# Performance work log

Hardware: AMD Instinct MI355X
Metric: run time of the kernel (lower is better)

## Reference

```python
import jax, jax.numpy as jnp
import numpy as np

DEFAULT_MASK_VALUE = -0.7 * float(jnp.finfo(jnp.dtype('float32')).max)


def setup_inputs() -> dict:
    key = jax.random.key(0)
    k1, k2, k3, k4 = jax.random.split(key, 4)
    B, T, NQ, NKV, D = 2, 2048, 32, 8, 128
    query = jax.random.normal(k1, (B, T, NQ, D), dtype=jnp.float32)
    k = jax.random.normal(k2, (B, T, NKV, D), dtype=jnp.float32)
    v = jax.random.normal(k3, (B, T, NKV, D), dtype=jnp.float32)
    # packed-sequence segment ids: sorted small ints so segments are contiguous
    decoder_segment_ids = jnp.sort(jax.random.randint(k4, (B, T), 0, 4), axis=-1).astype(jnp.int32)
    return {"query": query, "key": k, "value": v, "decoder_segment_ids": decoder_segment_ids}


def _generate_attention_mask(q_seq_len, kv_seq_len, decoder_segment_ids):
    # segment mask: [b, 1, 1, t, s]
    seg = (decoder_segment_ids[:, :, None] == decoder_segment_ids[:, None, :])[:, None, None, :, :]
    # causal mask: [1, 1, 1, t, s]
    row = jax.lax.broadcasted_iota(jnp.int32, (q_seq_len, kv_seq_len), 0)
    col = jax.lax.broadcasted_iota(jnp.int32, (q_seq_len, kv_seq_len), 1)
    causal = (col <= row)[None, None, None, :, :]
    mask = jnp.logical_and(seg, causal)
    return jnp.where(mask, 0.0, DEFAULT_MASK_VALUE)


def _apply_mask_to_logits(logits, mask):
    return jnp.where(mask >= DEFAULT_MASK_VALUE * 0.5, logits, DEFAULT_MASK_VALUE)


def reference(query, key, value, decoder_segment_ids):
    b, t, n, d = query.shape
    n_kv = key.shape[2]
    g = n // n_kv  # query heads per kv head (GQA)
    q = query.reshape(b, t, n_kv, g, d)
    # qk product (no internal sqrt(d) scaling, matching AttentionOp.qk_product)
    logits = jnp.einsum('btkgd,bskd->bkgts', q, key)  # [b, n_kv, g, t, s]
    mask = _generate_attention_mask(t, key.shape[1], decoder_segment_ids)
    logits = _apply_mask_to_logits(logits, mask)
    weights = jax.nn.softmax(logits, axis=-1).astype(query.dtype)
    out = jnp.einsum('bkgts,bskd->btkgd', weights, value)
    return out.reshape(b, t, n, d)
```

## Files before the change

kernel.cpp:

```cpp
#include <hip/hip_runtime.h>


typedef __bf16 bf16x8 __attribute__((ext_vector_type(8)));
typedef __bf16 bf16x2 __attribute__((ext_vector_type(2)));
typedef _Float16 f16x8 __attribute__((ext_vector_type(8)));
typedef float f32x4 __attribute__((ext_vector_type(4)));
typedef unsigned int uint2v __attribute__((ext_vector_type(2)));

#define B_   2
#define T_   2048
#define NQ_  32
#define NKV_ 8
#define D_   128

#define MASKV (-3.0e38f)
#define LOG2E 1.44269504f
#define TILE_US 8192
#define WS_TILES_BYTES ((size_t)B_ * NKV_ * (T_ / 32) * TILE_US * 2)
#define WS_NEED (WS_TILES_BYTES + (size_t)B_ * T_ * 4)

static __device__ __forceinline__ unsigned short f2bf(float x) {
    union { float f; unsigned int u; } c; c.f = x;
    unsigned int r = c.u + 0x7fffu + ((c.u >> 16) & 1u);
    return (unsigned short)(r >> 16);
}

union U8  { unsigned short us[8]; bf16x8 v; };
union H8  { _Float16 h[8]; f16x8 v; };
union PKW { bf16x2 h; unsigned int u; };
union PA4 { unsigned int u[4]; bf16x8 v; };

static __device__ __forceinline__ void pl32swap(unsigned int& a, unsigned int& b) {
#if __has_builtin(__builtin_amdgcn_permlane32_swap)
    uint2v t = __builtin_amdgcn_permlane32_swap(a, b, false, false);
    a = t.x; b = t.y;
#else
    asm("s_nop 1\n\tv_permlane32_swap_b32 %0, %1" : "+v"(a), "+v"(b));
#endif
}
static __device__ __forceinline__ void pl16swap(unsigned int& a, unsigned int& b) {
#if __has_builtin(__builtin_amdgcn_permlane16_swap)
    uint2v t = __builtin_amdgcn_permlane16_swap(a, b, false, false);
    a = t.x; b = t.y;
#else
    asm("s_nop 1\n\tv_permlane16_swap_b32 %0, %1" : "+v"(a), "+v"(b));
#endif
}

__global__ __launch_bounds__(256)
void prep(const float* __restrict__ kg, const float* __restrict__ vg,
          unsigned short* __restrict__ ws)
{
    const int tid = threadIdx.x;
    const int st  = blockIdx.x;
    const int kvh = blockIdx.y;
    const int b   = blockIdx.z;
    unsigned short* base = ws + ((size_t)((b * NKV_ + kvh) * (T_ / 32) + st)) * TILE_US;

    #pragma unroll
    for (int it = 0; it < 2; ++it) {
        int task = tid + it * 256;
        int r = task >> 4, c16 = task & 15;
        const float* kp = kg + (((size_t)(b * T_ + st * 32 + r)) * NKV_ + kvh) * D_ + c16 * 8;
        H8 hu;
        #pragma unroll
        for (int j = 0; j < 8; ++j) hu.h[j] = (_Float16)kp[j];
        int c = c16 >> 2, qd = c16 & 3, hi = r >> 4, ln = r & 15;
        int slot = (c * 2 + hi) * 64 + qd * 16 + ln;
        *(f16x8*)(base + slot * 8) = hu.v;
    }
    #pragma unroll
    for (int it = 0; it < 2; ++it) {
        int task = tid + it * 256;
        int d = task & 127, sc = task >> 7;
        const float* vp = vg + (((size_t)(b * T_ + st * 32 + sc * 8)) * NKV_ + kvh) * D_ + d;
        U8 pk;
        #pragma unroll
        for (int j = 0; j < 8; ++j) pk.us[j] = f2bf(vp[j * (NKV_ * D_)]);
        int slot = (d >> 4) * 64 + sc * 16 + (d & 15);
        *(bf16x8*)(base + 4096 + slot * 8) = pk.v;
    }
}

__global__ __launch_bounds__(256)
void prep_sstart(const int* __restrict__ seg, int* __restrict__ sstart)
{
    int idx = blockIdx.x * 256 + threadIdx.x;
    int b = idx >> 11, t = idx & (T_ - 1);
    const int* sb = seg + b * T_;
    int target = sb[t];
    int lo = 0, hi = t;
    while (lo < hi) { int mid = (lo + hi) >> 1; if (sb[mid] < target) lo = mid + 1; else hi = mid; }
    sstart[idx] = lo;
}

__global__ __launch_bounds__(256)
void attn_fwd(const float* __restrict__ qg,
              const int* __restrict__ sstart,
              const unsigned short* __restrict__ ws,
              float* __restrict__ outg)
{
    const int tid  = threadIdx.x;
    const int wave = tid >> 6;
    const int lane = tid & 63;
    const int qd   = lane >> 4;
    const int ln   = lane & 15;

    const int kvh  = blockIdx.x;
    const int head = kvh * 4 + wave;
    const int j    = blockIdx.y;
    const int b    = blockIdx.z;

    const unsigned short* wsbase =
        ws + ((size_t)((b * NKV_ + kvh) * (T_ / 32))) * TILE_US + lane * 8;

#define LOADKV(KB, VB, tl) do {                                                \
        const unsigned short* _tb = wsbase + (size_t)(tl) * TILE_US;           \
        _Pragma("unroll")                                                      \
        for (int _c = 0; _c < 4; ++_c) {                                       \
            KB[_c][0] = *(const f16x8*)(_tb + (_c * 2 + 0) * 512);             \
            KB[_c][1] = *(const f16x8*)(_tb + (_c * 2 + 1) * 512);             \
        }                                                                      \
        _Pragma("unroll")                                                      \
        for (int _s = 0; _s < 8; ++_s)                                         \
            VB[_s] = *(const bf16x8*)(_tb + 4096 + _s * 512);                  \
    } while (0)

#define COMPUTE(KB, VB, TL) do {                                               \
        const int _s0 = (TL) * 32;                                             \
        f32x4 S0 = {0.f,0.f,0.f,0.f}, S1 = {0.f,0.f,0.f,0.f};                  \
        __builtin_amdgcn_s_setprio(1);                                         \
        _Pragma("unroll")                                                      \
        for (int c = 0; c < 4; ++c) {                                          \
            S0 = __builtin_amdgcn_mfma_f32_16x16x32_f16(KB[c][0], qh[c], S0,0,0,0); \
            S1 = __builtin_amdgcn_mfma_f32_16x16x32_f16(KB[c][1], qh[c], S1,0,0,0); \
            S0 = __builtin_amdgcn_mfma_f32_16x16x32_f16(KB[c][0], ql[c], S0,0,0,0); \
            S1 = __builtin_amdgcn_mfma_f32_16x16x32_f16(KB[c][1], ql[c], S1,0,0,0); \
        }                                                                      \
        __builtin_amdgcn_s_setprio(0);                                         \
        float p0[4], p1[4];                                                    \
        if (_s0 >= wave_rs_max && _s0 + 31 <= wave_row_min) {                  \
            _Pragma("unroll")                                                  \
            for (int r = 0; r < 4; ++r) {                                      \
                p0[r] = exp2f(S0[r]);                                          \
                p1[r] = exp2f(S1[r]);                                          \
            }                                                                  \
        } else {                                                               \
            _Pragma("unroll")                                                  \
            for (int r = 0; r < 4; ++r) {                                      \
                int kv0 = _s0 + qd * 4 + r;                                    \
                int kv1 = kv0 + 16;                                            \
                float sv0 = (kv0 >= rs_l && kv0 <= trow_l) ? S0[r] : MASKV;    \
                float sv1 = (kv1 >= rs_l && kv1 <= trow_l) ? S1[r] : MASKV;    \
                p0[r] = exp2f(sv0);                                            \
                p1[r] = exp2f(sv1);                                            \
            }                                                                  \
        }                                                                      \
        l_lane += (p0[0] + p0[1]) + (p0[2] + p0[3])                            \
                + (p1[0] + p1[1]) + (p1[2] + p1[3]);                           \
        PKW c0, c1, c2, c3;                                                    \
        c0.h = (bf16x2){(__bf16)p0[0], (__bf16)p0[1]};                         \
        c1.h = (bf16x2){(__bf16)p0[2], (__bf16)p0[3]};                         \
        c2.h = (bf16x2){(__bf16)p1[0], (__bf16)p1[1]};                         \
        c3.h = (bf16x2){(__bf16)p1[2], (__bf16)p1[3]};                         \
        unsigned int w0 = c0.u, w1 = c1.u, w2 = c2.u, w3 = c3.u;               \
        pl32swap(w0, w2); pl32swap(w1, w3);                                    \
        pl16swap(w0, w2); pl16swap(w1, w3);                                    \
        PA4 pw; pw.u[0] = w0; pw.u[1] = w1; pw.u[2] = w2; pw.u[3] = w3;        \
        bf16x8 pa = pw.v;                                                      \
        __builtin_amdgcn_s_setprio(1);                                         \
        _Pragma("unroll")                                                      \
        for (int sub = 0; sub < 8; ++sub)                                      \
            O[sub] = __builtin_amdgcn_mfma_f32_16x16x32_bf16(pa, VB[sub], O[sub],0,0,0); \
        __builtin_amdgcn_s_setprio(0);                                         \
    } while (0)

    for (int phase = 0; phase < 2; ++phase) {
        const int chunk = (phase == 0) ? (2 * (int)gridDim.y - 1 - j) : j;
        const int t0 = chunk * 16;

        f16x8 qh[4], ql[4];
        {
            const float* qrow =
                qg + (((size_t)(b * T_ + (t0 + ln)) * NQ_) + head) * D_;
            #pragma unroll
            for (int c = 0; c < 4; ++c) {
                float4 a  = *(const float4*)(qrow + c * 32 + qd * 8);
                float4 b2 = *(const float4*)(qrow + c * 32 + qd * 8 + 4);
                float xs[8] = {a.x, a.y, a.z, a.w, b2.x, b2.y, b2.z, b2.w};
                H8 hu, lu;
                #pragma unroll
                for (int jj = 0; jj < 8; ++jj) {
                    float x = xs[jj] * LOG2E;
                    _Float16 h = (_Float16)x;
                    hu.h[jj] = h;
                    lu.h[jj] = (_Float16)(x - (float)h);
                }
                qh[c] = hu.v; ql[c] = lu.v;
            }
        }

        const int trow_l = t0 + ln;
        const int rs_l   = sstart[b * T_ + trow_l];
        const int wave_rs_max  = sstart[b * T_ + t0 + 15];
        const int wave_row_min = t0;

        const int tile0   = sstart[b * T_ + t0] >> 5;
        const int n_tiles = ((t0 + 15) >> 5) + 1;

        f32x4 O[8];
        #pragma unroll
        for (int k = 0; k < 8; ++k) O[k] = (f32x4){0.f, 0.f, 0.f, 0.f};
        float l_lane = 0.f;

        f16x8  kA[4][2], kB_[4][2];
        bf16x8 vA[8], vB_[8];

        int t = tile0;
        LOADKV(kA, vA, t);
        while (t + 1 < n_tiles) {
            LOADKV(kB_, vB_, t + 1);
            COMPUTE(kA, vA, t);
            if (t + 2 < n_tiles) LOADKV(kA, vA, t + 2);
            COMPUTE(kB_, vB_, t + 1);
            t += 2;
        }
        if (t < n_tiles) COMPUTE(kA, vA, t);

        float l = l_lane;
        l += __shfl_xor(l, 16);
        l += __shfl_xor(l, 32);
        const float invl = 1.0f / l;
        int trow[4];
        float inv[4];
        #pragma unroll
        for (int r = 0; r < 4; ++r) {
            trow[r] = t0 + qd * 4 + r;
            inv[r]  = __shfl(invl, qd * 4 + r);
        }
        #pragma unroll
        for (int sub = 0; sub < 8; ++sub) {
            #pragma unroll
            for (int r = 0; r < 4; ++r) {
                outg[(((size_t)(b * T_ + trow[r]) * NQ_) + head) * D_ + sub * 16 + ln] =
                    O[sub][r] * inv[r];
            }
        }
    }

#undef LOADKV
#undef COMPUTE
}

#define KSTR 136
#define VSTR 40
#define PSTR 40
static __device__ __forceinline__ float bf2f(unsigned short h) {
    union { unsigned int u; float f; } c; c.u = (unsigned int)h << 16; return c.f;
}
__global__ __launch_bounds__(256)
void attn_fwd_fb(const float* __restrict__ qg,
                 const float* __restrict__ kg,
                 const float* __restrict__ vg,
                 const int* __restrict__ seg,
                 float* __restrict__ outg)
{
    __shared__ unsigned short sKh[32 * KSTR];
    __shared__ unsigned short sKl[32 * KSTR];
    __shared__ unsigned short sVt[128 * VSTR];
    __shared__ unsigned short sP[4][16 * PSTR];

    const int tid  = threadIdx.x;
    const int wave = tid >> 6;
    const int lane = tid & 63;
    const int qd   = lane >> 4;
    const int ln   = lane & 15;
    const int t0   = ((int)gridDim.x - 1 - (int)blockIdx.x) * 64;
    const int head = blockIdx.y;
    const int kvh  = head >> 2;
    const int b    = blockIdx.z;

    bf16x8 qh[4], ql[4];
    {
        const float* qrow =
            qg + (((size_t)(b * T_ + (t0 + wave * 16 + ln)) * NQ_) + head) * D_;
        #pragma unroll
        for (int c = 0; c < 4; ++c) {
            float4 a  = *(const float4*)(qrow + c * 32 + qd * 8);
            float4 b2 = *(const float4*)(qrow + c * 32 + qd * 8 + 4);
            float xs[8] = {a.x, a.y, a.z, a.w, b2.x, b2.y, b2.z, b2.w};
            U8 hu, lu;
            #pragma unroll
            for (int j = 0; j < 8; ++j) {
                unsigned short h = f2bf(xs[j]);
                hu.us[j] = h;
                lu.us[j] = f2bf(xs[j] - bf2f(h));
            }
            qh[c] = hu.v; ql[c] = lu.v;
        }
    }
    const int* sb = seg + (size_t)b * T_;
    int qseg[4];
    #pragma unroll
    for (int r = 0; r < 4; ++r) qseg[r] = sb[t0 + wave * 16 + qd * 4 + r];
    int tile0;
    {
        int target = sb[t0];
        int lo = 0, hi = t0;
        while (lo < hi) { int mid = (lo + hi) >> 1; if (sb[mid] < target) lo = mid + 1; else hi = mid; }
        tile0 = lo >> 5;
    }
    f32x4 O[8];
    #pragma unroll
    for (int i = 0; i < 8; ++i) O[i] = (f32x4){0.f, 0.f, 0.f, 0.f};
    float m_prev[4], l_lane[4];
    #pragma unroll
    for (int r = 0; r < 4; ++r) { m_prev[r] = MASKV; l_lane[r] = 0.f; }
    const int n_tiles = t0 / 32 + 2;

    for (int tile = tile0; tile < n_tiles; ++tile) {
        const int s0 = tile * 32;
        __syncthreads();
        #pragma unroll
        for (int it = 0; it < 2; ++it) {
            int task = tid + it * 256;
            int r = task >> 4, d = (task & 15) * 8;
            const float* kp = kg + (((size_t)(b * T_ + s0 + r) * NKV_) + kvh) * D_ + d;
            float4 a  = *(const float4*)(kp);
            float4 b2 = *(const float4*)(kp + 4);
            float xs[8] = {a.x, a.y, a.z, a.w, b2.x, b2.y, b2.z, b2.w};
            U8 hu, lu;
            #pragma unroll
            for (int j = 0; j < 8; ++j) {
                unsigned short h = f2bf(xs[j]);
                hu.us[j] = h;
                lu.us[j] = f2bf(xs[j] - bf2f(h));
            }
            *(bf16x8*)(sKh + r * KSTR + d) = hu.v;
            *(bf16x8*)(sKl + r * KSTR + d) = lu.v;
        }
        #pragma unroll
        for (int it = 0; it < 2; ++it) {
            int task = tid + it * 256;
            int d = task & 127, sg = task >> 7;
            const float* vp = vg + (((size_t)(b * T_ + s0 + sg * 8) * NKV_) + kvh) * D_ + d;
            U8 pk;
            #pragma unroll
            for (int j = 0; j < 8; ++j) pk.us[j] = f2bf(vp[j * (NKV_ * D_)]);
            *(bf16x8*)(sVt + d * VSTR + sg * 8) = pk.v;
        }
        __syncthreads();

        f32x4 S0 = {0.f,0.f,0.f,0.f}, S1 = {0.f,0.f,0.f,0.f};
        #pragma unroll
        for (int c = 0; c < 4; ++c) {
            bf16x8 kh0 = *(const bf16x8*)(sKh + ln * KSTR + c * 32 + qd * 8);
            bf16x8 kh1 = *(const bf16x8*)(sKh + (16 + ln) * KSTR + c * 32 + qd * 8);
            bf16x8 kl0 = *(const bf16x8*)(sKl + ln * KSTR + c * 32 + qd * 8);
            bf16x8 kl1 = *(const bf16x8*)(sKl + (16 + ln) * KSTR + c * 32 + qd * 8);
            S0 = __builtin_amdgcn_mfma_f32_16x16x32_bf16(qh[c], kh0, S0, 0, 0, 0);
            S1 = __builtin_amdgcn_mfma_f32_16x16x32_bf16(qh[c], kh1, S1, 0, 0, 0);
            S0 = __builtin_amdgcn_mfma_f32_16x16x32_bf16(qh[c], kl0, S0, 0, 0, 0);
            S1 = __builtin_amdgcn_mfma_f32_16x16x32_bf16(qh[c], kl1, S1, 0, 0, 0);
            S0 = __builtin_amdgcn_mfma_f32_16x16x32_bf16(ql[c], kh0, S0, 0, 0, 0);
            S1 = __builtin_amdgcn_mfma_f32_16x16x32_bf16(ql[c], kh1, S1, 0, 0, 0);
        }
        const int ks0 = sb[s0 + ln];
        const int ks1 = sb[s0 + 16 + ln];
        float p0[4], p1[4], alpha[4];
        #pragma unroll
        for (int r = 0; r < 4; ++r) {
            const int trow = t0 + wave * 16 + qd * 4 + r;
            float s0v = ((s0 + ln <= trow) && (ks0 == qseg[r])) ? S0[r] : MASKV;
            float s1v = ((s0 + 16 + ln <= trow) && (ks1 == qseg[r])) ? S1[r] : MASKV;
            float mx = fmaxf(s0v, s1v);
            mx = fmaxf(mx, __shfl_xor(mx, 1));
            mx = fmaxf(mx, __shfl_xor(mx, 2));
            mx = fmaxf(mx, __shfl_xor(mx, 4));
            mx = fmaxf(mx, __shfl_xor(mx, 8));
            const float mn = fmaxf(m_prev[r], mx);
            alpha[r] = __expf(m_prev[r] - mn);
            p0[r] = __expf(s0v - mn);
            p1[r] = __expf(s1v - mn);
            l_lane[r] = alpha[r] * l_lane[r] + p0[r] + p1[r];
            m_prev[r] = mn;
        }
        #pragma unroll
        for (int i = 0; i < 8; ++i) {
            O[i][0] *= alpha[0]; O[i][1] *= alpha[1];
            O[i][2] *= alpha[2]; O[i][3] *= alpha[3];
        }
        {
            unsigned short* pw = sP[wave] + (qd * 4) * PSTR + ln;
            #pragma unroll
            for (int r = 0; r < 4; ++r) {
                pw[r * PSTR]      = f2bf(p0[r]);
                pw[r * PSTR + 16] = f2bf(p1[r]);
            }
        }
        asm volatile("s_waitcnt lgkmcnt(0)" ::: "memory");
        bf16x8 pa = *(const bf16x8*)(sP[wave] + ln * PSTR + qd * 8);
        #pragma unroll
        for (int sub = 0; sub < 8; ++sub) {
            bf16x8 bv = *(const bf16x8*)(sVt + (sub * 16 + ln) * VSTR + qd * 8);
            O[sub] = __builtin_amdgcn_mfma_f32_16x16x32_bf16(pa, bv, O[sub], 0, 0, 0);
        }
    }
    float inv[4];
    #pragma unroll
    for (int r = 0; r < 4; ++r) {
        float l = l_lane[r];
        l += __shfl_xor(l, 1);
        l += __shfl_xor(l, 2);
        l += __shfl_xor(l, 4);
        l += __shfl_xor(l, 8);
        inv[r] = 1.0f / l;
    }
    #pragma unroll
    for (int sub = 0; sub < 8; ++sub) {
        #pragma unroll
        for (int r = 0; r < 4; ++r) {
            const int trow = t0 + wave * 16 + qd * 4 + r;
            outg[(((size_t)(b * T_ + trow) * NQ_) + head) * D_ + sub * 16 + ln] =
                O[sub][r] * inv[r];
        }
    }
}

extern "C" void kernel_launch(void* const* d_in, const int* in_sizes, int n_in,
                              void* d_out, int out_size, void* d_ws, size_t ws_size,
                              hipStream_t stream) {
    const float* q  = (const float*)d_in[0];
    const float* k  = (const float*)d_in[1];
    const float* v  = (const float*)d_in[2];
    const int*   sg = (const int*)d_in[3];
    float*       o  = (float*)d_out;
    if (ws_size >= WS_NEED) {
        unsigned short* ws = (unsigned short*)d_ws;
        int* sstart = (int*)((char*)d_ws + WS_TILES_BYTES);
        prep<<<dim3(T_ / 32, NKV_, B_), dim3(256), 0, stream>>>(k, v, ws);
        prep_sstart<<<dim3(B_ * T_ / 256), dim3(256), 0, stream>>>(sg, sstart);
        attn_fwd<<<dim3(NKV_, T_ / 32, B_), dim3(256), 0, stream>>>(q, sstart, ws, o);
    } else {
        attn_fwd_fb<<<dim3(T_ / 64, NQ_, B_), dim3(256), 0, stream>>>(q, k, v, sg, o);
    }
}
```

Baseline: 193.5 us.

## Process two 16-row query groups per wave to reuse each K/V tile

Each wave now handles 32 query rows as two 16-row groups that share every loaded K/V tile, which halves the tile loads per query row. The grid's T dimension is halved to match, and the fast unmasked path is taken only when the whole 32-row block is unmasked. This doubles the accumulator and Q registers, which may lower occupancy, and halves the number of blocks launched. It also coarsens the causal boundary, so more diagonal tiles go through the masked path.

Measured after the change: 205.7 us. 1.06x slower.

```diff
diff --git a/kernel.cpp b/kernel.cpp
--- a/kernel.cpp
+++ b/kernel.cpp
@@ -126,20 +126,19 @@
             VB[_s] = *(const bf16x8*)(_tb + 4096 + _s * 512);                  \
     } while (0)
 
-#define COMPUTE(KB, VB, TL) do {                                               \
-        const int _s0 = (TL) * 32;                                             \
+#define QKPV(QH, QL, OO, LL, RS_L, TROW_L, KB, VB, FAST) do {                  \
         f32x4 S0 = {0.f,0.f,0.f,0.f}, S1 = {0.f,0.f,0.f,0.f};                  \
         __builtin_amdgcn_s_setprio(1);                                         \
         _Pragma("unroll")                                                      \
         for (int c = 0; c < 4; ++c) {                                          \
-            S0 = __builtin_amdgcn_mfma_f32_16x16x32_f16(KB[c][0], qh[c], S0,0,0,0); \
-            S1 = __builtin_amdgcn_mfma_f32_16x16x32_f16(KB[c][1], qh[c], S1,0,0,0); \
-            S0 = __builtin_amdgcn_mfma_f32_16x16x32_f16(KB[c][0], ql[c], S0,0,0,0); \
-            S1 = __builtin_amdgcn_mfma_f32_16x16x32_f16(KB[c][1], ql[c], S1,0,0,0); \
+            S0 = __builtin_amdgcn_mfma_f32_16x16x32_f16(KB[c][0], QH[c], S0,0,0,0); \
+            S1 = __builtin_amdgcn_mfma_f32_16x16x32_f16(KB[c][1], QH[c], S1,0,0,0); \
+            S0 = __builtin_amdgcn_mfma_f32_16x16x32_f16(KB[c][0], QL[c], S0,0,0,0); \
+            S1 = __builtin_amdgcn_mfma_f32_16x16x32_f16(KB[c][1], QL[c], S1,0,0,0); \
         }                                                                      \
         __builtin_amdgcn_s_setprio(0);                                         \
         float p0[4], p1[4];                                                    \
-        if (_s0 >= wave_rs_max && _s0 + 31 <= wave_row_min) {                  \
+        if (FAST) {                                                            \
             _Pragma("unroll")                                                  \
             for (int r = 0; r < 4; ++r) {                                      \
                 p0[r] = exp2f(S0[r]);                                          \
@@ -150,14 +149,14 @@
             for (int r = 0; r < 4; ++r) {                                      \
                 int kv0 = _s0 + qd * 4 + r;                                    \
                 int kv1 = kv0 + 16;                                            \
-                float sv0 = (kv0 >= rs_l && kv0 <= trow_l) ? S0[r] : MASKV;    \
-                float sv1 = (kv1 >= rs_l && kv1 <= trow_l) ? S1[r] : MASKV;    \
+                float sv0 = (kv0 >= (RS_L) && kv0 <= (TROW_L)) ? S0[r] : MASKV;\
+                float sv1 = (kv1 >= (RS_L) && kv1 <= (TROW_L)) ? S1[r] : MASKV;\
                 p0[r] = exp2f(sv0);                                            \
                 p1[r] = exp2f(sv1);                                            \
             }                                                                  \
         }                                                                      \
-        l_lane += (p0[0] + p0[1]) + (p0[2] + p0[3])                            \
-                + (p1[0] + p1[1]) + (p1[2] + p1[3]);                           \
+        LL += (p0[0] + p0[1]) + (p0[2] + p0[3])                                \
+            + (p1[0] + p1[1]) + (p1[2] + p1[3]);                               \
         PKW c0, c1, c2, c3;                                                    \
         c0.h = (bf16x2){(__bf16)p0[0], (__bf16)p0[1]};                         \
         c1.h = (bf16x2){(__bf16)p0[2], (__bf16)p0[3]};                         \
@@ -171,18 +170,26 @@
         __builtin_amdgcn_s_setprio(1);                                         \
         _Pragma("unroll")                                                      \
         for (int sub = 0; sub < 8; ++sub)                                      \
-            O[sub] = __builtin_amdgcn_mfma_f32_16x16x32_bf16(pa, VB[sub], O[sub],0,0,0); \
+            OO[sub] = __builtin_amdgcn_mfma_f32_16x16x32_bf16(pa, VB[sub], OO[sub],0,0,0); \
         __builtin_amdgcn_s_setprio(0);                                         \
     } while (0)
 
+#define COMPUTE(KB, VB, TL) do {                                               \
+        const int _s0 = (TL) * 32;                                             \
+        const bool fastall = (_s0 >= wave_rs_max) && (_s0 + 31 <= t0);         \
+        QKPV(qh0, ql0, O0, l0, rs0_l, trow0_l, KB, VB, fastall);               \
+        QKPV(qh1, ql1, O1, l1, rs1_l, trow1_l, KB, VB, fastall);               \
+    } while (0)
+
     for (int phase = 0; phase < 2; ++phase) {
         const int chunk = (phase == 0) ? (2 * (int)gridDim.y - 1 - j) : j;
-        const int t0 = chunk * 16;
-
-        f16x8 qh[4], ql[4];
-        {
+        const int t0 = chunk * 32;
+
+        f16x8 qh0[4], ql0[4], qh1[4], ql1[4];
+        #pragma unroll
+        for (int g = 0; g < 2; ++g) {
             const float* qrow =
-                qg + (((size_t)(b * T_ + (t0 + ln)) * NQ_) + head) * D_;
+                qg + (((size_t)(b * T_ + (t0 + g * 16 + ln)) * NQ_) + head) * D_;
             #pragma unroll
             for (int c = 0; c < 4; ++c) {
                 float4 a  = *(const float4*)(qrow + c * 32 + qd * 8);
@@ -196,22 +203,27 @@
                     hu.h[jj] = h;
                     lu.h[jj] = (_Float16)(x - (float)h);
                 }
-                qh[c] = hu.v; ql[c] = lu.v;
-            }
-        }
-
-        const int trow_l = t0 + ln;
-        const int rs_l   = sstart[b * T_ + trow_l];
-        const int wave_rs_max  = sstart[b * T_ + t0 + 15];
-        const int wave_row_min = t0;
+                if (g == 0) { qh0[c] = hu.v; ql0[c] = lu.v; }
+                else        { qh1[c] = hu.v; ql1[c] = lu.v; }
+            }
+        }
+
+        const int trow0_l = t0 + ln;
+        const int trow1_l = t0 + 16 + ln;
+        const int rs0_l   = sstart[b * T_ + trow0_l];
+        const int rs1_l   = sstart[b * T_ + trow1_l];
+        const int wave_rs_max = sstart[b * T_ + t0 + 31];
 
         const int tile0   = sstart[b * T_ + t0] >> 5;
-        const int n_tiles = ((t0 + 15) >> 5) + 1;
-
-        f32x4 O[8];
-        #pragma unroll
-        for (int k = 0; k < 8; ++k) O[k] = (f32x4){0.f, 0.f, 0.f, 0.f};
-        float l_lane = 0.f;
+        const int n_tiles = chunk + 1;
+
+        f32x4 O0[8], O1[8];
+        #pragma unroll
+        for (int k = 0; k < 8; ++k) {
+            O0[k] = (f32x4){0.f, 0.f, 0.f, 0.f};
+            O1[k] = (f32x4){0.f, 0.f, 0.f, 0.f};
+        }
+        float l0 = 0.f, l1 = 0.f;
 
         f16x8  kA[4][2], kB_[4][2];
         bf16x8 vA[8], vB_[8];
@@ -227,28 +239,33 @@
         }
         if (t < n_tiles) COMPUTE(kA, vA, t);
 
-        float l = l_lane;
-        l += __shfl_xor(l, 16);
-        l += __shfl_xor(l, 32);
-        const float invl = 1.0f / l;
-        int trow[4];
-        float inv[4];
-        #pragma unroll
-        for (int r = 0; r < 4; ++r) {
-            trow[r] = t0 + qd * 4 + r;
-            inv[r]  = __shfl(invl, qd * 4 + r);
-        }
-        #pragma unroll
-        for (int sub = 0; sub < 8; ++sub) {
+        #pragma unroll
+        for (int g = 0; g < 2; ++g) {
+            float l = (g == 0) ? l0 : l1;
+            l += __shfl_xor(l, 16);
+            l += __shfl_xor(l, 32);
+            const float invl = 1.0f / l;
+            int trow[4];
+            float inv[4];
             #pragma unroll
             for (int r = 0; r < 4; ++r) {
-                outg[(((size_t)(b * T_ + trow[r]) * NQ_) + head) * D_ + sub * 16 + ln] =
-                    O[sub][r] * inv[r];
+                trow[r] = t0 + g * 16 + qd * 4 + r;
+                inv[r]  = __shfl(invl, qd * 4 + r);
+            }
+            #pragma unroll
+            for (int sub = 0; sub < 8; ++sub) {
+                #pragma unroll
+                for (int r = 0; r < 4; ++r) {
+                    float ov = (g == 0) ? O0[sub][r] : O1[sub][r];
+                    outg[(((size_t)(b * T_ + trow[r]) * NQ_) + head) * D_ + sub * 16 + ln] =
+                        ov * inv[r];
+                }
             }
         }
     }
 
 #undef LOADKV
+#undef QKPV
 #undef COMPUTE
 }
 
@@ -440,7 +457,7 @@
         int* sstart = (int*)((char*)d_ws + WS_TILES_BYTES);
         prep<<<dim3(T_ / 32, NKV_, B_), dim3(256), 0, stream>>>(k, v, ws);
         prep_sstart<<<dim3(B_ * T_ / 256), dim3(256), 0, stream>>>(sg, sstart);
-        attn_fwd<<<dim3(NKV_, T_ / 32, B_), dim3(256), 0, stream>>>(q, sstart, ws, o);
+        attn_fwd<<<dim3(NKV_, T_ / 64, B_), dim3(256), 0, stream>>>(q, sstart, ws, o);
     } else {
         attn_fwd_fb<<<dim3(T_ / 64, NQ_, B_), dim3(256), 0, stream>>>(q, k, v, sg, o);
     }
```
